# Performance work log

Hardware: AMD Instinct MI355X
Metric: run time of the kernel (lower is better)

## Reference

```python
import jax, jax.numpy as jnp
import numpy as np

INPUT_DIM = 1024
HIDDEN_DIM = 2048
NUM_BLOCKS = 8
BLOCK_SIZE = HIDDEN_DIM // NUM_BLOCKS
BATCH = 2048


def setup_inputs() -> dict:
    key = jax.random.key(0)
    ks = jax.random.split(key, 6)
    # PyTorch GRUCell init: uniform(-1/sqrt(hidden_size), 1/sqrt(hidden_size))
    bound = 1.0 / np.sqrt(BLOCK_SIZE)
    u = lambda k, shape: jax.random.uniform(k, shape, jnp.float32, -bound, bound)
    return {
        "input": jax.random.normal(ks[0], (BATCH, INPUT_DIM), jnp.float32),
        "hidden": jax.random.normal(ks[1], (BATCH, HIDDEN_DIM), jnp.float32),
        # stacked per-block GRUCell params (block-diagonal structure)
        "W_ih": u(ks[2], (NUM_BLOCKS, 3 * BLOCK_SIZE, INPUT_DIM)),
        "W_hh": u(ks[3], (NUM_BLOCKS, 3 * BLOCK_SIZE, BLOCK_SIZE)),
        "b_ih": u(ks[4], (NUM_BLOCKS, 3 * BLOCK_SIZE)),
        "b_hh": u(ks[5], (NUM_BLOCKS, 3 * BLOCK_SIZE)),
    }


def reference(input, hidden, W_ih, W_hh, b_ih, b_hh):
    B = input.shape[0]
    nb, g3, bs = W_hh.shape  # [num_blocks, 3*block_size, block_size]
    hb = hidden.reshape(B, nb, bs)                      # [B, nb, bs]
    # input-to-gate and hidden-to-gate projections, batched over blocks
    gi = jnp.einsum("bi,ngi->bng", input, W_ih) + b_ih  # [B, nb, 3*bs]
    gh = jnp.einsum("bns,ngs->bng", hb, W_hh) + b_hh    # [B, nb, 3*bs]
    i_r, i_z, i_n = jnp.split(gi, 3, axis=-1)
    h_r, h_z, h_n = jnp.split(gh, 3, axis=-1)
    r = jax.nn.sigmoid(i_r + h_r)
    z = jax.nn.sigmoid(i_z + h_z)
    n = jnp.tanh(i_n + r * h_n)
    new_h = (1.0 - z) * n + z * hb                      # [B, nb, bs]
    return new_h.reshape(B, nb * bs)
```

## Files before the change

### kernel.cpp

```cpp
#include <hip/hip_runtime.h>
#include <hip/hip_bf16.h>
#include <type_traits>

typedef __attribute__((ext_vector_type(4))) float f32x4;
typedef __attribute__((ext_vector_type(8))) short bf16x8;

template <int V> using ic = std::integral_constant<int, V>;

static constexpr int B_   = 2048;
static constexpr int IN_  = 1024;
static constexpr int HID_ = 2048;
static constexpr int NB_  = 8;
static constexpr int BS_  = 256;
static constexpr int G3_  = 768;

__device__ __forceinline__ unsigned short f2bf(float f) {
  unsigned u = __builtin_bit_cast(unsigned, f);
  u = (u + 0x7FFFu + ((u >> 16) & 1u)) >> 16;
  return (unsigned short)u;
}

__global__ __launch_bounds__(256, 2) void gru_mfma(
    const float* __restrict__ xf,
    const float* __restrict__ hf,
    const float* __restrict__ Wih,
    const float* __restrict__ Whh,
    const float* __restrict__ b_ih,
    const float* __restrict__ b_hh,
    float* __restrict__ out)
{
  __shared__ __align__(16) char lds[2][40960];

  const int t    = threadIdx.x;
  const int lane = t & 63;
  const int wid  = t >> 6;
  const int wm   = wid >> 1;
  const int wn   = wid & 1;

  const int bid = blockIdx.x;
  const int swz = (bid & 7) * 64 + (bid >> 3);
  const int mrow0 = (swz & 15) * 128;
  const int ct    = swz >> 4;
  const int n     = ct >> 2;
  const int s0    = (ct & 3) * 64;

  int arow[4], acol[4];
#pragma unroll
  for (int p = 0; p < 4; ++p) {
    int op = p * 4096 + t * 16;
    int ol = op ^ (((op >> 7) & 7) << 4);
    arow[p] = ol >> 7;
    acol[p] = (ol & 127) >> 1;
  }
  int wgrow[6], wcol[6];
#pragma unroll
  for (int q = 0; q < 6; ++q) {
    int op = q * 4096 + t * 16;
    int ol = op ^ (((op >> 7) & 7) << 4);
    int wr = ol >> 7;
    wgrow[q] = n * G3_ + (wr >> 6) * BS_ + s0 + (wr & 63);
    wcol[q]  = (ol & 127) >> 1;
  }

  f32x4 acc[4][4][2] = {};
  float4 sa[4][2];
  float4 sw[3][2];

  auto issueA = [&](int t2) {
#pragma unroll
    for (int p = 0; p < 4; ++p) {
      const float* src = (t2 < 16)
        ? xf + (size_t)(mrow0 + arow[p]) * IN_  + t2 * 64 + acol[p]
        : hf + (size_t)(mrow0 + arow[p]) * HID_ + n * BS_ + (t2 - 16) * 64 + acol[p];
      sa[p][0] = *reinterpret_cast<const float4*>(src);
      sa[p][1] = *reinterpret_cast<const float4*>(src + 4);
    }
  };
  auto issueW = [&](int t2, int q0) {
#pragma unroll
    for (int j = 0; j < 3; ++j) {
      const int q = q0 + j;
      const float* src = (t2 < 16)
        ? Wih + (size_t)wgrow[q] * IN_ + t2 * 64 + wcol[q]
        : Whh + (size_t)wgrow[q] * BS_ + (t2 - 16) * 64 + wcol[q];
      sw[j][0] = *reinterpret_cast<const float4*>(src);
      sw[j][1] = *reinterpret_cast<const float4*>(src + 4);
    }
  };
  auto pack = [](const float4 (&v)[2]) {
    union { bf16x8 b; unsigned short s[8]; } u;
    u.s[0] = f2bf(v[0].x); u.s[1] = f2bf(v[0].y);
    u.s[2] = f2bf(v[0].z); u.s[3] = f2bf(v[0].w);
    u.s[4] = f2bf(v[1].x); u.s[5] = f2bf(v[1].y);
    u.s[6] = f2bf(v[1].z); u.s[7] = f2bf(v[1].w);
    return u.b;
  };
  auto writeA = [&](char* buf) {
#pragma unroll
    for (int p = 0; p < 4; ++p)
      *reinterpret_cast<bf16x8*>(buf + p * 4096 + t * 16) = pack(sa[p]);
  };
  auto writeW = [&](char* buf, int q0) {
#pragma unroll
    for (int j = 0; j < 3; ++j)
      *reinterpret_cast<bf16x8*>(buf + 16384 + (q0 + j) * 4096 + t * 16) = pack(sw[j]);
  };

  auto loadA = [&](const char* buf, bf16x8 (&af)[2][4]) {
#pragma unroll
    for (int ksub = 0; ksub < 2; ++ksub)
#pragma unroll
      for (int mi = 0; mi < 4; ++mi) {
        int ar  = wm * 64 + mi * 16 + (lane & 15);
        int off = ar * 128 + ksub * 64 + ((lane >> 4) * 16);
        off ^= (ar & 7) << 4;
        af[ksub][mi] = *reinterpret_cast<const bf16x8*>(buf + off);
      }
  };
  auto loadW = [&](const char* buf, int g, bf16x8 (&wf)[2][2]) {
#pragma unroll
    for (int ksub = 0; ksub < 2; ++ksub)
#pragma unroll
      for (int ni = 0; ni < 2; ++ni) {
        int wr  = g * 64 + wn * 32 + ni * 16 + (lane & 15);
        int off = wr * 128 + ksub * 64 + ((lane >> 4) * 16);
        off ^= (wr & 7) << 4;
        wf[ksub][ni] = *reinterpret_cast<const bf16x8*>(buf + 16384 + off);
      }
  };
  auto mfmaSet = [&](auto setc, bf16x8 (&af)[2][4], bf16x8 (&wf)[2][2]) {
    constexpr int set = decltype(setc)::value;
#pragma unroll
    for (int ksub = 0; ksub < 2; ++ksub)
#pragma unroll
      for (int mi = 0; mi < 4; ++mi)
#pragma unroll
        for (int ni = 0; ni < 2; ++ni)
          acc[set][mi][ni] = __builtin_amdgcn_mfma_f32_16x16x32_bf16(
              af[ksub][mi], wf[ksub][ni], acc[set][mi][ni], 0, 0, 0);
  };

  issueA(0);
  issueW(0, 0);
  writeA((char*)lds[0]);
  writeW((char*)lds[0], 0);
  issueW(0, 3);
  writeW((char*)lds[0], 3);
  __syncthreads();

#pragma unroll
  for (int tt = 0; tt < 20; ++tt) {
    char* cur = (char*)lds[tt & 1];
    char* oth = (char*)lds[(tt & 1) ^ 1];
    bf16x8 af[2][4], wf[2][2];

    if (tt < 19) issueA(tt + 1);
    loadA(cur, af);
    loadW(cur, 0, wf);
    mfmaSet(ic<0>{}, af, wf);
    if (tt < 19) { writeA(oth); issueW(tt + 1, 0); }
    loadW(cur, 1, wf);
    mfmaSet(ic<1>{}, af, wf);
    if (tt < 19) { writeW(oth, 0); issueW(tt + 1, 3); }
    loadW(cur, 2, wf);
    if (tt < 16) mfmaSet(ic<2>{}, af, wf);
    else         mfmaSet(ic<3>{}, af, wf);
    if (tt < 19) writeW(oth, 3);
    __syncthreads();
  }

#pragma unroll
  for (int ni = 0; ni < 2; ++ni) {
    int scol = s0 + wn * 32 + ni * 16 + (lane & 15);
    float br_i = b_ih[n * G3_ + 0 * BS_ + scol];
    float bz_i = b_ih[n * G3_ + 1 * BS_ + scol];
    float bn_i = b_ih[n * G3_ + 2 * BS_ + scol];
    float br_h = b_hh[n * G3_ + 0 * BS_ + scol];
    float bz_h = b_hh[n * G3_ + 1 * BS_ + scol];
    float bn_h = b_hh[n * G3_ + 2 * BS_ + scol];
    int gcol = n * BS_ + scol;
#pragma unroll
    for (int mi = 0; mi < 4; ++mi) {
#pragma unroll
      for (int i = 0; i < 4; ++i) {
        int row = mrow0 + wm * 64 + mi * 16 + (lane >> 4) * 4 + i;
        float hprev = hf[(size_t)row * HID_ + gcol];
        float rr = acc[0][mi][ni][i] + br_i + br_h;
        float zz = acc[1][mi][ni][i] + bz_i + bz_h;
        float r  = 1.f / (1.f + __expf(-rr));
        float z  = 1.f / (1.f + __expf(-zz));
        float ng = tanhf(acc[2][mi][ni][i] + bn_i + r * (acc[3][mi][ni][i] + bn_h));
        out[(size_t)row * HID_ + gcol] = (1.f - z) * ng + z * hprev;
      }
    }
  }
}

extern "C" void kernel_launch(void* const* d_in, const int* in_sizes, int n_in,
                              void* d_out, int out_size, void* d_ws, size_t ws_size,
                              hipStream_t stream) {
  const float* x   = (const float*)d_in[0];
  const float* h   = (const float*)d_in[1];
  const float* Wih = (const float*)d_in[2];
  const float* Whh = (const float*)d_in[3];
  const float* bih = (const float*)d_in[4];
  const float* bhh = (const float*)d_in[5];
  float* out = (float*)d_out;
  (void)d_ws; (void)ws_size;

  gru_mfma<<<512, 256, 0, stream>>>(x, h, Wih, Whh, bih, bhh, out);
}
```

Measured before the change: 58.53 us.

## Rebalance prefetch batches, use hardware bf16 pack, add setprio and sched barriers

The global-to-LDS prefetch now runs in two batches (A plus two W chunks, then four W chunks) instead of three. This issues more loads earlier and reduces the number of write/issue points that interleave with the MFMA phases. The software round-to-nearest bf16 conversion is replaced by the v_cvt_pk_bf16_f32 instruction, which packs two values at once. MFMA sections are wrapped in s_setprio, and sched_barriers pin the instruction order. Together these aim to cut VALU conversion cost and overlap memory with compute better, at the cost of more staging registers, which could spill or hurt occupancy at two blocks per CU.

```diff
diff --git a/kernel.cpp b/kernel.cpp
--- a/kernel.cpp
+++ b/kernel.cpp
@@ -14,10 +14,10 @@
 static constexpr int BS_  = 256;
 static constexpr int G3_  = 768;
 
-__device__ __forceinline__ unsigned short f2bf(float f) {
-  unsigned u = __builtin_bit_cast(unsigned, f);
-  u = (u + 0x7FFFu + ((u >> 16) & 1u)) >> 16;
-  return (unsigned short)u;
+__device__ __forceinline__ unsigned cvtpk(float lo, float hi) {
+  unsigned r;
+  asm("v_cvt_pk_bf16_f32 %0, %1, %2" : "=v"(r) : "v"(lo), "v"(hi));
+  return r;
 }
 
 __global__ __launch_bounds__(256, 2) void gru_mfma(
@@ -63,47 +63,56 @@
   }
 
   f32x4 acc[4][4][2] = {};
-  float4 sa[4][2];
-  float4 sw[3][2];
-
-  auto issueA = [&](int t2) {
+  float4 s1[6][2];
+  float4 s2[4][2];
+
+  auto issueB1 = [&](int t2) {
 #pragma unroll
     for (int p = 0; p < 4; ++p) {
       const float* src = (t2 < 16)
         ? xf + (size_t)(mrow0 + arow[p]) * IN_  + t2 * 64 + acol[p]
         : hf + (size_t)(mrow0 + arow[p]) * HID_ + n * BS_ + (t2 - 16) * 64 + acol[p];
-      sa[p][0] = *reinterpret_cast<const float4*>(src);
-      sa[p][1] = *reinterpret_cast<const float4*>(src + 4);
-    }
-  };
-  auto issueW = [&](int t2, int q0) {
-#pragma unroll
-    for (int j = 0; j < 3; ++j) {
-      const int q = q0 + j;
+      s1[p][0] = *reinterpret_cast<const float4*>(src);
+      s1[p][1] = *reinterpret_cast<const float4*>(src + 4);
+    }
+#pragma unroll
+    for (int q = 0; q < 2; ++q) {
       const float* src = (t2 < 16)
         ? Wih + (size_t)wgrow[q] * IN_ + t2 * 64 + wcol[q]
         : Whh + (size_t)wgrow[q] * BS_ + (t2 - 16) * 64 + wcol[q];
-      sw[j][0] = *reinterpret_cast<const float4*>(src);
-      sw[j][1] = *reinterpret_cast<const float4*>(src + 4);
-    }
-  };
-  auto pack = [](const float4 (&v)[2]) {
-    union { bf16x8 b; unsigned short s[8]; } u;
-    u.s[0] = f2bf(v[0].x); u.s[1] = f2bf(v[0].y);
-    u.s[2] = f2bf(v[0].z); u.s[3] = f2bf(v[0].w);
-    u.s[4] = f2bf(v[1].x); u.s[5] = f2bf(v[1].y);
-    u.s[6] = f2bf(v[1].z); u.s[7] = f2bf(v[1].w);
-    return u.b;
-  };
-  auto writeA = [&](char* buf) {
+      s1[4 + q][0] = *reinterpret_cast<const float4*>(src);
+      s1[4 + q][1] = *reinterpret_cast<const float4*>(src + 4);
+    }
+  };
+  auto issueB2 = [&](int t2) {
+#pragma unroll
+    for (int j = 0; j < 4; ++j) {
+      const int q = 2 + j;
+      const float* src = (t2 < 16)
+        ? Wih + (size_t)wgrow[q] * IN_ + t2 * 64 + wcol[q]
+        : Whh + (size_t)wgrow[q] * BS_ + (t2 - 16) * 64 + wcol[q];
+      s2[j][0] = *reinterpret_cast<const float4*>(src);
+      s2[j][1] = *reinterpret_cast<const float4*>(src + 4);
+    }
+  };
+  auto pack8 = [&](const float4& a, const float4& b) {
+    union { unsigned u[4]; bf16x8 v; } r;
+    r.u[0] = cvtpk(a.x, a.y); r.u[1] = cvtpk(a.z, a.w);
+    r.u[2] = cvtpk(b.x, b.y); r.u[3] = cvtpk(b.z, b.w);
+    return r.v;
+  };
+  auto writeB1 = [&](char* buf) {
 #pragma unroll
     for (int p = 0; p < 4; ++p)
-      *reinterpret_cast<bf16x8*>(buf + p * 4096 + t * 16) = pack(sa[p]);
-  };
-  auto writeW = [&](char* buf, int q0) {
-#pragma unroll
-    for (int j = 0; j < 3; ++j)
-      *reinterpret_cast<bf16x8*>(buf + 16384 + (q0 + j) * 4096 + t * 16) = pack(sw[j]);
+      *reinterpret_cast<bf16x8*>(buf + p * 4096 + t * 16) = pack8(s1[p][0], s1[p][1]);
+#pragma unroll
+    for (int q = 0; q < 2; ++q)
+      *reinterpret_cast<bf16x8*>(buf + 16384 + q * 4096 + t * 16) = pack8(s1[4 + q][0], s1[4 + q][1]);
+  };
+  auto writeB2 = [&](char* buf) {
+#pragma unroll
+    for (int j = 0; j < 4; ++j)
+      *reinterpret_cast<bf16x8*>(buf + 16384 + (2 + j) * 4096 + t * 16) = pack8(s2[j][0], s2[j][1]);
   };
 
   auto loadA = [&](const char* buf, bf16x8 (&af)[2][4]) {
@@ -130,6 +139,7 @@
   };
   auto mfmaSet = [&](auto setc, bf16x8 (&af)[2][4], bf16x8 (&wf)[2][2]) {
     constexpr int set = decltype(setc)::value;
+    __builtin_amdgcn_s_setprio(1);
 #pragma unroll
     for (int ksub = 0; ksub < 2; ++ksub)
 #pragma unroll
@@ -138,14 +148,13 @@
         for (int ni = 0; ni < 2; ++ni)
           acc[set][mi][ni] = __builtin_amdgcn_mfma_f32_16x16x32_bf16(
               af[ksub][mi], wf[ksub][ni], acc[set][mi][ni], 0, 0, 0);
-  };
-
-  issueA(0);
-  issueW(0, 0);
-  writeA((char*)lds[0]);
-  writeW((char*)lds[0], 0);
-  issueW(0, 3);
-  writeW((char*)lds[0], 3);
+    __builtin_amdgcn_s_setprio(0);
+  };
+
+  issueB1(0);
+  writeB1((char*)lds[0]);
+  issueB2(0);
+  writeB2((char*)lds[0]);
   __syncthreads();
 
 #pragma unroll
@@ -154,18 +163,21 @@
     char* oth = (char*)lds[(tt & 1) ^ 1];
     bf16x8 af[2][4], wf[2][2];
 
-    if (tt < 19) issueA(tt + 1);
+    if (tt < 19) issueB1(tt + 1);
+    __builtin_amdgcn_sched_barrier(0);
     loadA(cur, af);
     loadW(cur, 0, wf);
     mfmaSet(ic<0>{}, af, wf);
-    if (tt < 19) { writeA(oth); issueW(tt + 1, 0); }
+    __builtin_amdgcn_sched_barrier(0);
+    if (tt < 19) { writeB1(oth); issueB2(tt + 1); }
+    __builtin_amdgcn_sched_barrier(0);
     loadW(cur, 1, wf);
     mfmaSet(ic<1>{}, af, wf);
-    if (tt < 19) { writeW(oth, 0); issueW(tt + 1, 3); }
     loadW(cur, 2, wf);
     if (tt < 16) mfmaSet(ic<2>{}, af, wf);
     else         mfmaSet(ic<3>{}, af, wf);
-    if (tt < 19) writeW(oth, 3);
+    __builtin_amdgcn_sched_barrier(0);
+    if (tt < 19) writeB2(oth);
     __syncthreads();
   }
 
```

After: 55.60 us. 5.0% less time.
